# Kernel optimization log

Hardware: AMD Instinct MI355X
Metric: run time of the kernel (lower is better)

## Reference

```python
import jax, jax.numpy as jnp
import numpy as np

WINDOW_SIZE, SM, PS = 8, 2, 2  # window_size, spatial_merge_size, patch_size
SMU = SM * SM  # spatial_merge_unit


def _window_index(grid_thw):
    """Numpy port of get_window_index; returns permutation of arange(S)."""
    vmws = WINDOW_SIZE // SM // PS  # 2
    out, wid = [], 0
    for t, h, w in grid_thw:
        lh, lw = h // SM, w // SM
        idx = np.arange(t * lh * lw).reshape(t, lh, lw)
        ph = vmws - lh % vmws
        pw = vmws - lw % vmws
        nh, nw = (lh + ph) // vmws, (lw + pw) // vmws
        pad = np.full((t, lh + ph, lw + pw), -100, dtype=np.int64)
        pad[:, :lh, :lw] = idx
        pad = pad.reshape(t, nh, vmws, nw, vmws).transpose(0, 1, 3, 2, 4).reshape(-1)
        out.append(pad[pad != -100] + wid)
        wid += t * lh * lw
    return np.concatenate(out).astype(np.int32)


def setup_inputs() -> dict:
    key = jax.random.key(0)
    ks = jax.random.split(key, 5)
    B, T, C, H = 1, 16384, 1280, 16
    D = C // H  # 80
    grid_thw = np.array([[1, 256, 256]], dtype=np.int64)  # llm grid 128x128 -> S=16384
    wi = _window_index(grid_thw)
    x = jax.random.normal(ks[0], (B, T, C), jnp.float32)
    cos = jax.random.normal(ks[1], (B * T, 1, D), jnp.float32)
    sin = jax.random.normal(ks[2], (B * T, 1, D), jnp.float32)
    W_qkv = jax.random.normal(ks[3], (C, 3 * C), jnp.float32) * (C ** -0.5)
    W_proj = jax.random.normal(ks[4], (C, C), jnp.float32) * (C ** -0.5)
    # each window: (vmws*vmws) merged tokens * SMU patches = 16 tokens
    block_size = (WINDOW_SIZE // SM // PS) ** 2 * SMU
    return {"x": x, "cos": cos, "sin": sin, "W_qkv": W_qkv, "W_proj": W_proj,
            "window_index": jnp.asarray(wi), "block_size": block_size}


def reference(x, cos, sin, W_qkv, W_proj, window_index, block_size):
    B, T, C = x.shape
    S = B * T
    D = cos.shape[-1]
    H = C // D
    # window reorder (gather)
    xr = x.reshape(S, C)[window_index]
    qkv = (xr @ W_qkv).reshape(S, 3, H, D)
    q, k, v = qkv[:, 0], qkv[:, 1], qkv[:, 2]
    # module's (unusual) q/k mixing 'rotary'
    cw, sw = cos[window_index], sin[window_index]  # (S,1,D) broadcast over heads
    qr = q * cw + k * sw
    kr = k * cw - q * sw
    # block-diagonal attention: uniform 16-token windows -> reshape, no SxS mask
    nb = S // block_size
    qb = qr.reshape(nb, block_size, H, D)
    kb = kr.reshape(nb, block_size, H, D)
    vb = v.reshape(nb, block_size, H, D)
    att = jnp.einsum('bqhd,bkhd->bhqk', qb, kb) * (D ** -0.5)
    att = jax.nn.softmax(att, axis=-1)
    y = jnp.einsum('bhqk,bkhd->bqhd', att, vb).reshape(S, C)
    # undo window reorder
    y = y[jnp.argsort(window_index)]
    return y.reshape(B, T, C) @ W_proj
```

## Files before the change

kernel.cpp:

```cpp
#include <hip/hip_runtime.h>
#include <hip/hip_bf16.h>

#define S_TOK   16384
#define C_DIM   1280
#define C3_DIM  3840
#define H_DIM   16
#define D_DIM   80
#define BLK     16
#define PLANE_ELEMS ((size_t)S_TOK * C_DIM)

using u16x8  = __attribute__((ext_vector_type(8))) unsigned short;
using u16x4  = __attribute__((ext_vector_type(4))) unsigned short;
using bf16x8 = __attribute__((ext_vector_type(8))) __bf16;
using f32x4  = __attribute__((ext_vector_type(4))) float;

__device__ __forceinline__ unsigned short f2bf(float f) {
    return __bfloat16_as_ushort(__float2bfloat16(f));
}
__device__ __forceinline__ float bf2f(unsigned short u) {
    unsigned int x = (unsigned int)u << 16;
    return __builtin_bit_cast(float, x);
}
__device__ __forceinline__ void gload_lds16(const unsigned short* g, unsigned short* l) {
    __builtin_amdgcn_global_load_lds(
        (const __attribute__((address_space(1))) void*)g,
        (__attribute__((address_space(3))) void*)l, 16, 0, 0);
}

__global__ __launch_bounds__(256) void transpose_cvt(
    const float* __restrict__ W, unsigned short* __restrict__ WT, int K, int N)
{
    __shared__ float tile[32][33];
    const int n0 = blockIdx.x * 32, k0 = blockIdx.y * 32;
    const int tx = threadIdx.x & 31, ty = threadIdx.x >> 5;
#pragma unroll
    for (int i = ty; i < 32; i += 8)
        tile[i][tx] = W[(size_t)(k0 + i) * N + n0 + tx];
    __syncthreads();
#pragma unroll
    for (int i = ty; i < 32; i += 8)
        WT[(size_t)(n0 + i) * K + k0 + tx] = f2bf(tile[tx][i]);
}

__global__ __launch_bounds__(256) void gather_cvt(
    const float* __restrict__ x, const int* __restrict__ wi,
    unsigned short* __restrict__ xg)
{
    int idx = blockIdx.x * 256 + threadIdx.x;
    int s  = idx / 160;
    int c8 = (idx - s * 160) * 8;
    const float* src = x + (size_t)wi[s] * C_DIM + c8;
    f32x4 v0 = *(const f32x4*)src;
    f32x4 v1 = *(const f32x4*)(src + 4);
    u16x8 o;
    o[0]=f2bf(v0[0]); o[1]=f2bf(v0[1]); o[2]=f2bf(v0[2]); o[3]=f2bf(v0[3]);
    o[4]=f2bf(v1[0]); o[5]=f2bf(v1[1]); o[6]=f2bf(v1[2]); o[7]=f2bf(v1[3]);
    *(u16x8*)&xg[(size_t)s * C_DIM + c8] = o;
}

__global__ __launch_bounds__(256) void inv_perm(
    const int* __restrict__ wi, int* __restrict__ inv)
{
    int s = blockIdx.x * 256 + threadIdx.x;
    inv[wi[s]] = s;
}

#define TM 128
#define TN 128
#define BK 64

template<int OUTMODE, bool GATHER>
__global__ __launch_bounds__(256) void gemm_mfma(
    const unsigned short* __restrict__ A,
    const unsigned short* __restrict__ BT,
    void* __restrict__ Cp,
    const int* __restrict__ row_map,
    int N, int K)
{
    __shared__ __align__(16) unsigned short As[TM * BK];
    __shared__ __align__(16) unsigned short Bs[TN * BK];

    const int m0   = blockIdx.x * TM;
    const int n0   = blockIdx.y * TN;
    const int tid  = threadIdx.x;
    const int lane = tid & 63;
    const int wv   = tid >> 6;
    const int wm   = (wv >> 1) * 64;
    const int wn   = (wv & 1) * 64;
    const int lrow = lane & 15;
    const int quad = lane >> 4;

    int gr[4], nr[4], csw[4];
#pragma unroll
    for (int c = 0; c < 4; c++) {
        int ch = (wv * 4 + c) * 64 + lane;
        int r  = ch >> 3;
        csw[c] = ((ch & 7) ^ (r & 7)) << 3;
        gr[c]  = GATHER ? row_map[m0 + r] : (m0 + r);
        nr[c]  = n0 + r;
    }

    int aoff[4], asw[4], boff[4], bsw[4];
#pragma unroll
    for (int t = 0; t < 4; t++) {
        int ra = wm + t * 16 + lrow;
        aoff[t] = ra << 7;  asw[t] = (ra & 7) << 4;
        int rb = wn + t * 16 + lrow;
        boff[t] = rb << 7;  bsw[t] = (rb & 7) << 4;
    }

    f32x4 acc[4][4];
#pragma unroll
    for (int i = 0; i < 4; i++)
#pragma unroll
        for (int j = 0; j < 4; j++)
            acc[i][j] = (f32x4){0.f, 0.f, 0.f, 0.f};

    for (int kt = 0; kt < K; kt += BK) {
#pragma unroll
        for (int c = 0; c < 4; c++)
            gload_lds16(A + (size_t)gr[c] * K + kt + csw[c],
                        As + (wv * 4 + c) * 512);
#pragma unroll
        for (int c = 0; c < 4; c++)
            gload_lds16(BT + (size_t)nr[c] * K + kt + csw[c],
                        Bs + (wv * 4 + c) * 512);
        __syncthreads();

#pragma unroll
        for (int ks = 0; ks < BK; ks += 32) {
            const int cb = (ks << 1) + (quad << 4);
            bf16x8 af[4], bfr[4];
#pragma unroll
            for (int mt = 0; mt < 4; mt++)
                af[mt] = *(const bf16x8*)((const char*)As +
                                          aoff[mt] + (cb ^ asw[mt]));
#pragma unroll
            for (int nt = 0; nt < 4; nt++)
                bfr[nt] = *(const bf16x8*)((const char*)Bs +
                                           boff[nt] + (cb ^ bsw[nt]));
#pragma unroll
            for (int mt = 0; mt < 4; mt++)
#pragma unroll
                for (int nt = 0; nt < 4; nt++)
                    acc[mt][nt] = __builtin_amdgcn_mfma_f32_16x16x32_bf16(
                        af[mt], bfr[nt], acc[mt][nt], 0, 0, 0);
        }
        __syncthreads();
    }

#pragma unroll
    for (int nt = 0; nt < 4; nt++) {
        const int cb = n0 + wn + nt * 16;
        unsigned short* pb = nullptr;
        if (OUTMODE == 2) {
            int which = cb / C_DIM;
            int hc    = cb - which * C_DIM;
            int h     = hc / D_DIM;
            int d0    = hc - h * D_DIM;
            pb = (unsigned short*)Cp + (size_t)which * PLANE_ELEMS
               + (size_t)h * S_TOK * D_DIM + d0 + lrow;
        }
#pragma unroll
        for (int mt = 0; mt < 4; mt++)
#pragma unroll
            for (int r = 0; r < 4; r++) {
                int row = m0 + wm + mt * 16 + quad * 4 + r;
                if (OUTMODE == 0)
                    ((float*)Cp)[(size_t)row * N + cb + lrow] = acc[mt][nt][r];
                else
                    pb[(size_t)row * D_DIM] = f2bf(acc[mt][nt][r]);
            }
    }
}

__global__ __launch_bounds__(256) void attn_v2(
    const unsigned short* __restrict__ planes,
    const float* __restrict__ cosp,
    const float* __restrict__ sinp,
    const int* __restrict__ wi,
    unsigned short* __restrict__ yw)
{
    __shared__ __align__(16) unsigned short Q_lds[4][16][88];
    __shared__ __align__(16) unsigned short K_lds[4][16][88];
    __shared__ __align__(16) unsigned short V_lds[4][1536];

    const int wave = threadIdx.x >> 6;
    const int lane = threadIdx.x & 63;
    const int b    = blockIdx.y;
    const int h    = blockIdx.x * 4 + wave;
    const int j16  = lane & 15;
    const int quad = lane >> 4;

    const unsigned short* Vsrc = planes + 2 * PLANE_ELEMS
        + ((size_t)h * S_TOK + b * BLK) * D_DIM;
    unsigned short* Vsl = &V_lds[wave][0];
#pragma unroll
    for (int c = 0; c < 3; c++)
        gload_lds16(Vsrc + c * 512 + lane * 8, Vsl + c * 512);

    const unsigned short* Qbase = planes + ((size_t)h * S_TOK + b * BLK) * D_DIM;
#pragma unroll
    for (int c = 0; c < 3; c++) {
        int ch = c * 64 + lane;
        if (ch < 160) {
            int r  = ch / 10;
            int d8 = (ch - r * 10) * 8;
            int crow = wi[b * BLK + r];
            const unsigned short* Qp = Qbase + (size_t)r * D_DIM + d8;
            u16x8 qv = *(const u16x8*)Qp;
            u16x8 kv = *(const u16x8*)(Qp + PLANE_ELEMS);
            const float* cp = cosp + (size_t)crow * D_DIM + d8;
            const float* sp = sinp + (size_t)crow * D_DIM + d8;
            f32x4 c0 = *(const f32x4*)cp, c1 = *(const f32x4*)(cp + 4);
            f32x4 s0 = *(const f32x4*)sp, s1 = *(const f32x4*)(sp + 4);
            u16x8 qo, ko;
#pragma unroll
            for (int j = 0; j < 8; j++) {
                float cw = (j < 4) ? c0[j] : c1[j - 4];
                float sw = (j < 4) ? s0[j] : s1[j - 4];
                float q = bf2f(qv[j]), k = bf2f(kv[j]);
                qo[j] = f2bf(q * cw + k * sw);
                ko[j] = f2bf(k * cw - q * sw);
            }
            *(u16x8*)&Q_lds[wave][r][d8] = qo;
            *(u16x8*)&K_lds[wave][r][d8] = ko;
        }
    }

    asm volatile("s_waitcnt vmcnt(0)" ::: "memory");
    __builtin_amdgcn_sched_barrier(0);

    const u16x8 zz = {0, 0, 0, 0, 0, 0, 0, 0};
    bf16x8 qf[3], kf[3];
#pragma unroll
    for (int s = 0; s < 3; s++) {
        int dcol = 32 * s + quad * 8;
        bool pad = (dcol >= D_DIM);
        int dc = pad ? 0 : dcol;
        u16x8 qv = *(const u16x8*)&Q_lds[wave][j16][dc];
        u16x8 kv = *(const u16x8*)&K_lds[wave][j16][dc];
        if (pad) { qv = zz; kv = zz; }
        qf[s] = __builtin_bit_cast(bf16x8, qv);
        kf[s] = __builtin_bit_cast(bf16x8, kv);
    }

    f32x4 sacc = (f32x4){0.f, 0.f, 0.f, 0.f};
#pragma unroll
    for (int s = 0; s < 3; s++)
        sacc = __builtin_amdgcn_mfma_f32_16x16x32_bf16(kf[s], qf[s], sacc, 0, 0, 0);

    const float scale = 0.11180339887498948f;
    float sc[4];
#pragma unroll
    for (int r = 0; r < 4; r++) sc[r] = sacc[r] * scale;
    float m = fmaxf(fmaxf(sc[0], sc[1]), fmaxf(sc[2], sc[3]));
    m = fmaxf(m, __shfl_xor(m, 16));
    m = fmaxf(m, __shfl_xor(m, 32));
    float e[4], sum = 0.f;
#pragma unroll
    for (int r = 0; r < 4; r++) { e[r] = __expf(sc[r] - m); sum += e[r]; }
    sum += __shfl_xor(sum, 16);
    sum += __shfl_xor(sum, 32);
    float inv = 1.f / sum;

    int sl = quad * 32 + j16;
    float pv0[4], pv1[4];
#pragma unroll
    for (int r = 0; r < 4; r++) pv0[r] = __shfl(e[r], sl & 63);
#pragma unroll
    for (int r = 0; r < 4; r++) pv1[r] = __shfl(e[r], (sl + 16) & 63);
    u16x8 pf;
#pragma unroll
    for (int r = 0; r < 4; r++) {
        pf[r]     = (quad < 2) ? f2bf(pv0[r]) : (unsigned short)0;
        pf[r + 4] = (quad < 2) ? f2bf(pv1[r]) : (unsigned short)0;
    }
    bf16x8 pfrag = __builtin_bit_cast(bf16x8, pf);

    u16x8 vf[5];
#pragma unroll
    for (int t = 0; t < 5; t++) {
#pragma unroll
        for (int e8 = 0; e8 < 8; e8++) {
            int kks = quad * 8 + e8;
            if (kks >= BLK) kks = e8;
            vf[t][e8] = Vsl[kks * D_DIM + t * 16 + j16];
        }
    }

    unsigned short* yrow = yw + (size_t)(b * BLK + j16) * C_DIM
                         + h * D_DIM + quad * 4;
#pragma unroll
    for (int t = 0; t < 5; t++) {
        f32x4 o = __builtin_amdgcn_mfma_f32_16x16x32_bf16(
            __builtin_bit_cast(bf16x8, vf[t]), pfrag,
            (f32x4){0.f, 0.f, 0.f, 0.f}, 0, 0, 0);
        u16x4 ov;
#pragma unroll
        for (int r = 0; r < 4; r++) ov[r] = f2bf(o[r] * inv);
        *(u16x4*)(yrow + t * 16) = ov;
    }
}

extern "C" void kernel_launch(void* const* d_in, const int* in_sizes, int n_in,
                              void* d_out, int out_size, void* d_ws, size_t ws_size,
                              hipStream_t stream)
{
    const float* x     = (const float*)d_in[0];
    const float* cosp  = (const float*)d_in[1];
    const float* sinp  = (const float*)d_in[2];
    const float* Wqkv  = (const float*)d_in[3];
    const float* Wproj = (const float*)d_in[4];
    const int*   wi    = (const int*)d_in[5];

    char* ws = (char*)d_ws;
    unsigned short* planes = (unsigned short*)ws;
    unsigned short* yw     = (unsigned short*)(ws + 125829120ull);
    unsigned short* wqkvT  = (unsigned short*)(ws + 167772160ull);
    unsigned short* wprojT = (unsigned short*)(ws + 177602560ull);
    unsigned short* xg     = (unsigned short*)(ws + 180879360ull);
    int*            inv    = (int*)(ws + 180879360ull);

    transpose_cvt<<<dim3(C3_DIM / 32, C_DIM / 32), 256, 0, stream>>>(
        Wqkv, wqkvT, C_DIM, C3_DIM);
    transpose_cvt<<<dim3(C_DIM / 32, C_DIM / 32), 256, 0, stream>>>(
        Wproj, wprojT, C_DIM, C_DIM);

    gather_cvt<<<S_TOK * 160 / 256, 256, 0, stream>>>(x, wi, xg);

    gemm_mfma<2, false><<<dim3(S_TOK / TM, C3_DIM / TN), 256, 0, stream>>>(
        xg, wqkvT, planes, nullptr, C3_DIM, C_DIM);

    inv_perm<<<S_TOK / 256, 256, 0, stream>>>(wi, inv);

    attn_v2<<<dim3(H_DIM / 4, S_TOK / BLK), 256, 0, stream>>>(
        planes, cosp, sinp, wi, yw);

    gemm_mfma<0, true><<<dim3(S_TOK / TM, C_DIM / TN), 256, 0, stream>>>(
        yw, wprojT, d_out, inv, C_DIM, C_DIM);
}
```

Before: 464.5 us.

## Replace 128x128 GEMM with double-buffered 256x256 tile MFMA GEMM

Both GEMMs now use a 512-thread kernel with 256x256 output tiles, so each wave computes a 128x64 sub-tile. The kernel double-buffers A/B tiles in LDS and issues async global-to-LDS loads two K-steps ahead. It interleaves MFMA groups with barriers and s_setprio so the loads overlap with compute. This is meant to raise arithmetic intensity and hide load latency. The cost is 128KB of LDS per block and heavy register use from 32 accumulators, and the projection GEMM launches only 320 blocks, which may leave CUs underused.

```diff
diff --git a/kernel.cpp b/kernel.cpp
--- a/kernel.cpp
+++ b/kernel.cpp
@@ -25,6 +25,10 @@
     __builtin_amdgcn_global_load_lds(
         (const __attribute__((address_space(1))) void*)g,
         (__attribute__((address_space(3))) void*)l, 16, 0, 0);
+}
+__device__ __forceinline__ bf16x8 lds_read_swz(const unsigned short* buf,
+                                               int off, int xr, int cb) {
+    return *(const bf16x8*)((const char*)buf + off + (cb ^ xr));
 }
 
 __global__ __launch_bounds__(256) void transpose_cvt(
@@ -65,111 +69,158 @@
     inv[wi[s]] = s;
 }
 
-#define TM 128
-#define TN 128
-#define BK 64
+#define BK2 64
 
 template<int OUTMODE, bool GATHER>
-__global__ __launch_bounds__(256) void gemm_mfma(
+__global__ __launch_bounds__(512, 2) void gemm256(
     const unsigned short* __restrict__ A,
     const unsigned short* __restrict__ BT,
     void* __restrict__ Cp,
     const int* __restrict__ row_map,
     int N, int K)
 {
-    __shared__ __align__(16) unsigned short As[TM * BK];
-    __shared__ __align__(16) unsigned short Bs[TN * BK];
-
-    const int m0   = blockIdx.x * TM;
-    const int n0   = blockIdx.y * TN;
+    __shared__ __align__(16) unsigned short AsB[2 * 16384];
+    __shared__ __align__(16) unsigned short BsB[2 * 16384];
+
+    const int m0   = blockIdx.x * 256;
+    const int n0   = blockIdx.y * 256;
     const int tid  = threadIdx.x;
     const int lane = tid & 63;
     const int wv   = tid >> 6;
-    const int wm   = (wv >> 1) * 64;
-    const int wn   = (wv & 1) * 64;
+    const int wm   = (wv >> 2) * 128;
+    const int wn   = (wv & 3) * 64;
     const int lrow = lane & 15;
     const int quad = lane >> 4;
 
-    int gr[4], nr[4], csw[4];
-#pragma unroll
-    for (int c = 0; c < 4; c++) {
-        int ch = (wv * 4 + c) * 64 + lane;
-        int r  = ch >> 3;
-        csw[c] = ((ch & 7) ^ (r & 7)) << 3;
-        gr[c]  = GATHER ? row_map[m0 + r] : (m0 + r);
-        nr[c]  = n0 + r;
-    }
-
-    int aoff[4], asw[4], boff[4], bsw[4];
-#pragma unroll
-    for (int t = 0; t < 4; t++) {
-        int ra = wm + t * 16 + lrow;
-        aoff[t] = ra << 7;  asw[t] = (ra & 7) << 4;
-        int rb = wn + t * 16 + lrow;
-        boff[t] = rb << 7;  bsw[t] = (rb & 7) << 4;
-    }
-
-    f32x4 acc[4][4];
-#pragma unroll
-    for (int i = 0; i < 4; i++)
+    const unsigned short* pa[4];
+    const unsigned short* pb[4];
+#pragma unroll
+    for (int i = 0; i < 4; i++) {
+        int gch = i * 512 + tid;
+        int r   = gch >> 3;
+        int c   = ((gch & 7) ^ (r & 7)) << 3;
+        int ga  = GATHER ? row_map[m0 + r] : (m0 + r);
+        pa[i] = A  + (size_t)ga * K + c;
+        pb[i] = BT + (size_t)(n0 + r) * K + c;
+    }
+
+    int aoff[8], axr[8], boff[4], bxr[4];
+#pragma unroll
+    for (int mt = 0; mt < 8; mt++) {
+        int r = wm + mt * 16 + lrow;
+        aoff[mt] = r << 7;  axr[mt] = (r & 7) << 4;
+    }
+#pragma unroll
+    for (int nt = 0; nt < 4; nt++) {
+        int r = wn + nt * 16 + lrow;
+        boff[nt] = r << 7;  bxr[nt] = (r & 7) << 4;
+    }
+
+    f32x4 acc[8][4];
+#pragma unroll
+    for (int i = 0; i < 8; i++)
 #pragma unroll
         for (int j = 0; j < 4; j++)
             acc[i][j] = (f32x4){0.f, 0.f, 0.f, 0.f};
 
-    for (int kt = 0; kt < K; kt += BK) {
-#pragma unroll
-        for (int c = 0; c < 4; c++)
-            gload_lds16(A + (size_t)gr[c] * K + kt + csw[c],
-                        As + (wv * 4 + c) * 512);
-#pragma unroll
-        for (int c = 0; c < 4; c++)
-            gload_lds16(BT + (size_t)nr[c] * K + kt + csw[c],
-                        Bs + (wv * 4 + c) * 512);
-        __syncthreads();
-
-#pragma unroll
-        for (int ks = 0; ks < BK; ks += 32) {
-            const int cb = (ks << 1) + (quad << 4);
-            bf16x8 af[4], bfr[4];
-#pragma unroll
-            for (int mt = 0; mt < 4; mt++)
-                af[mt] = *(const bf16x8*)((const char*)As +
-                                          aoff[mt] + (cb ^ asw[mt]));
+    const int NT = K >> 6;
+
+    auto stage = [&](int bsel, int koff) {
+#pragma unroll
+        for (int i = 0; i < 4; i++)
+            gload_lds16(pa[i] + koff, AsB + bsel * 16384 + i * 4096 + wv * 512);
+#pragma unroll
+        for (int i = 0; i < 4; i++)
+            gload_lds16(pb[i] + koff, BsB + bsel * 16384 + i * 4096 + wv * 512);
+    };
+
+    stage(0, 0);
+    stage(1, BK2);
+    asm volatile("s_waitcnt vmcnt(8)" ::: "memory");
+    __builtin_amdgcn_sched_barrier(0);
+    __builtin_amdgcn_s_barrier();
+    __builtin_amdgcn_sched_barrier(0);
+
+    int cur = 0;
+    for (int t = 0; t < NT; ++t) {
+        const unsigned short* Ac = AsB + cur * 16384;
+        const unsigned short* Bc = BsB + cur * 16384;
+        const int cb0 = quad << 4;
+        const int cb1 = 64 + (quad << 4);
+
+        bf16x8 a0[8], b0[4];
+#pragma unroll
+        for (int mt = 0; mt < 8; mt++) a0[mt] = lds_read_swz(Ac, aoff[mt], axr[mt], cb0);
+#pragma unroll
+        for (int nt = 0; nt < 4; nt++) b0[nt] = lds_read_swz(Bc, boff[nt], bxr[nt], cb0);
+        __builtin_amdgcn_s_setprio(1);
+#pragma unroll
+        for (int mt = 0; mt < 8; mt++)
 #pragma unroll
             for (int nt = 0; nt < 4; nt++)
-                bfr[nt] = *(const bf16x8*)((const char*)Bs +
-                                           boff[nt] + (cb ^ bsw[nt]));
-#pragma unroll
-            for (int mt = 0; mt < 4; mt++)
-#pragma unroll
-                for (int nt = 0; nt < 4; nt++)
-                    acc[mt][nt] = __builtin_amdgcn_mfma_f32_16x16x32_bf16(
-                        af[mt], bfr[nt], acc[mt][nt], 0, 0, 0);
+                acc[mt][nt] = __builtin_amdgcn_mfma_f32_16x16x32_bf16(
+                    a0[mt], b0[nt], acc[mt][nt], 0, 0, 0);
+        __builtin_amdgcn_s_setprio(0);
+
+        bf16x8 a1[8], b1[4];
+#pragma unroll
+        for (int mt = 0; mt < 8; mt++) a1[mt] = lds_read_swz(Ac, aoff[mt], axr[mt], cb1);
+#pragma unroll
+        for (int nt = 0; nt < 4; nt++) b1[nt] = lds_read_swz(Bc, boff[nt], bxr[nt], cb1);
+        __builtin_amdgcn_s_setprio(1);
+#pragma unroll
+        for (int mt = 0; mt < 4; mt++)
+#pragma unroll
+            for (int nt = 0; nt < 4; nt++)
+                acc[mt][nt] = __builtin_amdgcn_mfma_f32_16x16x32_bf16(
+                    a1[mt], b1[nt], acc[mt][nt], 0, 0, 0);
+        __builtin_amdgcn_s_setprio(0);
+        asm volatile("s_waitcnt lgkmcnt(0)" ::: "memory");
+        __builtin_amdgcn_sched_barrier(0);
+        __builtin_amdgcn_s_barrier();
+        __builtin_amdgcn_sched_barrier(0);
+
+        if (t + 2 < NT) stage(cur, (t + 2) * BK2);
+        __builtin_amdgcn_s_setprio(1);
+#pragma unroll
+        for (int mt = 4; mt < 8; mt++)
+#pragma unroll
+            for (int nt = 0; nt < 4; nt++)
+                acc[mt][nt] = __builtin_amdgcn_mfma_f32_16x16x32_bf16(
+                    a1[mt], b1[nt], acc[mt][nt], 0, 0, 0);
+        __builtin_amdgcn_s_setprio(0);
+        if (t + 2 < NT) {
+            asm volatile("s_waitcnt vmcnt(8)" ::: "memory");
+        } else if (t + 1 < NT) {
+            asm volatile("s_waitcnt vmcnt(0)" ::: "memory");
         }
-        __syncthreads();
+        __builtin_amdgcn_sched_barrier(0);
+        __builtin_amdgcn_s_barrier();
+        __builtin_amdgcn_sched_barrier(0);
+        cur ^= 1;
     }
 
 #pragma unroll
     for (int nt = 0; nt < 4; nt++) {
         const int cb = n0 + wn + nt * 16;
-        unsigned short* pb = nullptr;
+        unsigned short* pp = nullptr;
         if (OUTMODE == 2) {
             int which = cb / C_DIM;
             int hc    = cb - which * C_DIM;
             int h     = hc / D_DIM;
             int d0    = hc - h * D_DIM;
-            pb = (unsigned short*)Cp + (size_t)which * PLANE_ELEMS
+            pp = (unsigned short*)Cp + (size_t)which * PLANE_ELEMS
                + (size_t)h * S_TOK * D_DIM + d0 + lrow;
         }
 #pragma unroll
-        for (int mt = 0; mt < 4; mt++)
+        for (int mt = 0; mt < 8; mt++)
 #pragma unroll
             for (int r = 0; r < 4; r++) {
                 int row = m0 + wm + mt * 16 + quad * 4 + r;
                 if (OUTMODE == 0)
                     ((float*)Cp)[(size_t)row * N + cb + lrow] = acc[mt][nt][r];
                 else
-                    pb[(size_t)row * D_DIM] = f2bf(acc[mt][nt][r]);
+                    pp[(size_t)row * D_DIM] = f2bf(acc[mt][nt][r]);
             }
     }
 }
@@ -329,7 +380,7 @@
 
     gather_cvt<<<S_TOK * 160 / 256, 256, 0, stream>>>(x, wi, xg);
 
-    gemm_mfma<2, false><<<dim3(S_TOK / TM, C3_DIM / TN), 256, 0, stream>>>(
+    gemm256<2, false><<<dim3(S_TOK / 256, C3_DIM / 256), 512, 0, stream>>>(
         xg, wqkvT, planes, nullptr, C3_DIM, C_DIM);
 
     inv_perm<<<S_TOK / 256, 256, 0, stream>>>(wi, inv);
@@ -337,6 +388,6 @@
     attn_v2<<<dim3(H_DIM / 4, S_TOK / BLK), 256, 0, stream>>>(
         planes, cosp, sinp, wi, yw);
 
-    gemm_mfma<0, true><<<dim3(S_TOK / TM, C_DIM / TN), 256, 0, stream>>>(
+    gemm256<0, true><<<dim3(S_TOK / 256, C_DIM / 256), 512, 0, stream>>>(
         yw, wprojT, d_out, inv, C_DIM, C_DIM);
 }
```

After: 508.7 us. 9.5% more time.
